# Kernel optimization log

Measured on AMD Instinct MI355X. Metric: run time of the kernel, lower is better.

Reference implementation:

```python
import jax, jax.numpy as jnp
import numpy as np
import math

DK = 768  # latent_size used for the scale (not the per-head dim, matching the original)

def setup_inputs() -> dict:
    key = jax.random.key(0)
    k1, k2, k3 = jax.random.split(key, 3)
    B, H, S, D = 4, 12, 2048, 64
    queries = jax.random.normal(k1, (B, H, S, D), dtype=jnp.float32)
    keys = jax.random.normal(k2, (B, H, S, D), dtype=jnp.float32)
    values = jax.random.normal(k3, (B, S, H, D), dtype=jnp.float32)  # note [B,S,H,D] layout
    return {"queries": queries, "keys": keys, "values": values}

def reference(queries, keys, values):
    # scores: [B,H,S,S]
    scores = jnp.einsum('bhqd,bhkd->bhqk', queries, keys) / math.sqrt(DK)
    probs = jax.nn.softmax(scores, axis=3)
    v = jnp.transpose(values, (0, 2, 1, 3))  # [B,S,H,D] -> [B,H,S,D]
    return jnp.einsum('bhqk,bhkd->bhqd', probs, v)
```

## Files before the change

kernel.cpp:

```cpp
#include <hip/hip_runtime.h>

#define SQ 2048
#define DH 64
#define NH 12
#define NBH 48
#define QTILE 64
#define KTILE 64
#define NITER (SQ / KTILE)
#define NQT (SQ / QTILE)

typedef short short8 __attribute__((ext_vector_type(8)));
typedef float f32x4 __attribute__((ext_vector_type(4)));
typedef int   i32x4 __attribute__((ext_vector_type(4)));
typedef int   i32x2 __attribute__((ext_vector_type(2)));

#define MFMA16(a, b, c) __builtin_amdgcn_mfma_f32_16x16x32_bf16(a, b, c, 0, 0, 0)

typedef __attribute__((address_space(1))) const void* gas_ptr;
typedef __attribute__((address_space(3))) void* las_ptr;

__device__ __forceinline__ void load_lds16(const void* g, void* l) {
    __builtin_amdgcn_global_load_lds((gas_ptr)g, (las_ptr)l, 16, 0, 0);
}

__device__ __forceinline__ short f2bf(float f) {
    union { float f; unsigned u; } v;
    v.f = f;
    unsigned r = v.u + 0x7FFFu + ((v.u >> 16) & 1u);
    return (short)(r >> 16);
}

#if defined(__has_builtin) && __has_builtin(__builtin_amdgcn_cvt_pk_bf16_f32)
typedef __bf16 bf16x2_t __attribute__((ext_vector_type(2)));
__device__ __forceinline__ unsigned pk2bf(float a, float b) {
    bf16x2_t v = __builtin_amdgcn_cvt_pk_bf16_f32(a, b);
    union { bf16x2_t v; unsigned u; } c; c.v = v; return c.u;
}
#else
__device__ __forceinline__ unsigned pk2bf(float a, float b) {
    union { float f; unsigned u; } x, y; x.f = a; y.f = b;
    unsigned ra = x.u + 0x7FFFu + ((x.u >> 16) & 1u);
    unsigned rb = y.u + 0x7FFFu + ((y.u >> 16) & 1u);
    return (ra >> 16) | (rb & 0xFFFF0000u);
}
#endif

__global__ __launch_bounds__(256)
void convert_k(const float* __restrict__ K, short* __restrict__ Kb) {
    const size_t i = (size_t)(blockIdx.x * 256 + threadIdx.x) * 8;
    f32x4 a = *(const f32x4*)&K[i];
    f32x4 b = *(const f32x4*)&K[i + 4];
    unsigned o[4] = { pk2bf(a[0], a[1]), pk2bf(a[2], a[3]),
                      pk2bf(b[0], b[1]), pk2bf(b[2], b[3]) };
    *(i32x4*)&Kb[i] = *(i32x4*)o;
}

__global__ __launch_bounds__(256)
void transpose_v(const float* __restrict__ V, short* __restrict__ Vt) {
    __shared__ float Ls[64][68];
    const int bx = blockIdx.x;
    const int st = bx & 31;
    const int bh = bx >> 5;
    const int b = bh / NH, h = bh % NH;
    const int s0 = st * 64;
    const float* src = V + ((size_t)b * SQ * NH + (size_t)h) * DH;
    const int dg = threadIdx.x & 15;
    const int sl = threadIdx.x >> 4;
    #pragma unroll
    for (int p = 0; p < 4; ++p) {
        const int row = p * 16 + sl;
        *(f32x4*)&Ls[row][dg * 4] =
            *(const f32x4*)&src[(size_t)(s0 + row) * (NH * DH) + dg * 4];
    }
    __syncthreads();
    const int dr = threadIdx.x >> 2;
    const int sc = (threadIdx.x & 3) * 16;
    unsigned out[8];
    #pragma unroll
    for (int jj = 0; jj < 8; ++jj)
        out[jj] = pk2bf(Ls[sc + 2 * jj][dr], Ls[sc + 2 * jj + 1][dr]);
    short* dst = Vt + (size_t)bh * DH * SQ + (size_t)dr * SQ + s0 + sc;
    *(i32x4*)(dst)     = *(i32x4*)&out[0];
    *(i32x4*)(dst + 8) = *(i32x4*)&out[4];
}

__global__ __launch_bounds__(256)
void attn_fused_kernel(const float* __restrict__ Q,
                       const short* __restrict__ Kb,
                       const short* __restrict__ Vtg,
                       float* __restrict__ O) {
    __shared__ short Ks[KTILE * DH];
    __shared__ short Vs[DH * KTILE];
    __shared__ short Ps[QTILE][72];

    const int tid  = threadIdx.x;
    const int lane = tid & 63;
    const int w    = tid >> 6;
    const int n    = lane & 15;
    const int quad = lane >> 4;
    const int nx   = n & 7;

    const int bx = blockIdx.x;
    const int qt = bx & (NQT - 1);
    const int bh = bx >> 5;
    const int q0 = qt * QTILE;

    const float* Qb  = Q   + (size_t)bh * SQ * DH;
    const short* Kbh = Kb  + (size_t)bh * SQ * DH;
    const short* Vbh = Vtg + (size_t)bh * DH * SQ;
    float*       Ob  = O   + (size_t)bh * SQ * DH;

    const float qscale = 0.03608439182435161f * 1.4426950408889634f;

    short8 qf[2];
    {
        const int qrow = q0 + 16 * w + n;
        #pragma unroll
        for (int c = 0; c < 2; ++c) {
            const float* src = Qb + (size_t)qrow * DH + 32 * c + 8 * quad;
            short8 f;
            #pragma unroll
            for (int j = 0; j < 8; ++j) f[j] = f2bf(src[j] * qscale);
            qf[c] = f;
        }
    }

    const int gk = (lane & 7) ^ (lane >> 3);
    const int rr = w * 8 + (lane >> 3);
    const short* kg0 = Kbh + (size_t)rr * DH + gk * 8;
    const short* kg1 = kg0 + 32 * DH;
    const short* vg0 = Vbh + (size_t)rr * SQ + gk * 8;
    const short* vg1 = vg0 + 32 * SQ;
    char* ksb = (char*)Ks;
    char* vsb = (char*)Vs;

    const short* kb0p = &Ks[n * DH + ((quad ^ nx) * 8)];
    const short* kb1p = &Ks[n * DH + (((4 + quad) ^ nx) * 8)];
    const short* vb0p = &Vs[n * DH + ((quad ^ nx) * 8)];
    const short* vb1p = &Vs[n * DH + (((4 + quad) ^ nx) * 8)];

    f32x4 o[4];
    #pragma unroll
    for (int dt = 0; dt < 4; ++dt) o[dt] = (f32x4){0.f, 0.f, 0.f, 0.f};
    float lp[4] = {0.f, 0.f, 0.f, 0.f};

    for (int it = 0; it < NITER; ++it) {
        const size_t ko = (size_t)it * (KTILE * DH);
        const size_t vo = (size_t)it * KTILE;
        load_lds16(kg0 + ko, ksb + w * 1024);
        load_lds16(kg1 + ko, ksb + 4096 + w * 1024);
        load_lds16(vg0 + vo, vsb + w * 1024);
        load_lds16(vg1 + vo, vsb + 4096 + w * 1024);
        __syncthreads();

        f32x4 s[4];
        #pragma unroll
        for (int c = 0; c < 4; ++c) {
            short8 kb0 = *(const short8*)(kb0p + c * 1024);
            short8 kb1 = *(const short8*)(kb1p + c * 1024);
            f32x4 acc = (f32x4){0.f, 0.f, 0.f, 0.f};
            acc = MFMA16(kb0, qf[0], acc);
            acc = MFMA16(kb1, qf[1], acc);
            s[c] = acc;
        }

        #pragma unroll
        for (int c = 0; c < 4; ++c) {
            float p0 = __builtin_amdgcn_exp2f(s[c][0]);
            float p1 = __builtin_amdgcn_exp2f(s[c][1]);
            float p2 = __builtin_amdgcn_exp2f(s[c][2]);
            float p3 = __builtin_amdgcn_exp2f(s[c][3]);
            lp[c] += (p0 + p1) + (p2 + p3);
            i32x2 w2 = { (int)pk2bf(p0, p1), (int)pk2bf(p2, p3) };
            *(i32x2*)&Ps[16 * w + n][16 * c + 4 * quad] = w2;
        }

        #pragma unroll
        for (int kc = 0; kc < 2; ++kc) {
            short8 pa = *(const short8*)&Ps[16 * w + n][32 * kc + 8 * quad];
            const short* vbp = kc ? vb1p : vb0p;
            #pragma unroll
            for (int dt = 0; dt < 4; ++dt) {
                short8 vb = *(const short8*)(vbp + dt * 1024);
                o[dt] = MFMA16(pa, vb, o[dt]);
            }
        }
        __syncthreads();
    }

    float v = (lp[0] + lp[1]) + (lp[2] + lp[3]);
    v += __shfl_xor(v, 16, 64);
    v += __shfl_xor(v, 32, 64);
    const float linv = 1.0f / v;

    float rl[4];
    #pragma unroll
    for (int r = 0; r < 4; ++r) rl[r] = __shfl(linv, 4 * quad + r, 64);

    #pragma unroll
    for (int dt = 0; dt < 4; ++dt)
        #pragma unroll
        for (int r = 0; r < 4; ++r) {
            const int q = q0 + 16 * w + 4 * quad + r;
            Ob[(size_t)q * DH + 16 * dt + n] = o[dt][r] * rl[r];
        }
}

extern "C" void kernel_launch(void* const* d_in, const int* in_sizes, int n_in,
                              void* d_out, int out_size, void* d_ws, size_t ws_size,
                              hipStream_t stream) {
    const float* Q = (const float*)d_in[0];
    const float* K = (const float*)d_in[1];
    const float* V = (const float*)d_in[2];
    float* O = (float*)d_out;

    short* Kb  = (short*)d_ws;
    short* Vtg = Kb + (size_t)NBH * SQ * DH;

    convert_k<<<dim3(NBH * SQ * DH / 8 / 256), dim3(256), 0, stream>>>(K, Kb);
    transpose_v<<<dim3(NBH * 32), dim3(256), 0, stream>>>(V, Vtg);
    attn_fused_kernel<<<dim3(NBH * NQT), dim3(256), 0, stream>>>(Q, Kb, Vtg, O);
}
```

Measured before the change: 190.7 us.

## Use 32x32x16 MFMA with 128-row query tiles in fused attention

Each wave now owns 32 query rows instead of 16, so one block covers 128 queries, and the score and PV products use the 32x32x16 bf16 MFMA. Fragment indexing, the LDS swizzle offsets, the row-sum reduction and the output write are rewritten for the 32x32 accumulator layout. The aim is to halve how often each K/V tile is loaded per query and to raise MFMA work per LDS read. In exchange the grid has half as many blocks and each thread holds larger accumulators, which may lower occupancy.

After: 185.1 us. -2.9%, faster.

```diff
diff --git a/kernel.cpp b/kernel.cpp
--- a/kernel.cpp
+++ b/kernel.cpp
@@ -4,17 +4,18 @@
 #define DH 64
 #define NH 12
 #define NBH 48
-#define QTILE 64
+#define QTILE 128
 #define KTILE 64
 #define NITER (SQ / KTILE)
 #define NQT (SQ / QTILE)
 
 typedef short short8 __attribute__((ext_vector_type(8)));
-typedef float f32x4 __attribute__((ext_vector_type(4)));
+typedef float f32x4  __attribute__((ext_vector_type(4)));
+typedef float f32x16 __attribute__((ext_vector_type(16)));
 typedef int   i32x4 __attribute__((ext_vector_type(4)));
 typedef int   i32x2 __attribute__((ext_vector_type(2)));
 
-#define MFMA16(a, b, c) __builtin_amdgcn_mfma_f32_16x16x32_bf16(a, b, c, 0, 0, 0)
+#define MFMA32(a, b, c) __builtin_amdgcn_mfma_f32_32x32x16_bf16(a, b, c, 0, 0, 0)
 
 typedef __attribute__((address_space(1))) const void* gas_ptr;
 typedef __attribute__((address_space(3))) void* las_ptr;
@@ -96,13 +97,13 @@
     const int tid  = threadIdx.x;
     const int lane = tid & 63;
     const int w    = tid >> 6;
-    const int n    = lane & 15;
-    const int quad = lane >> 4;
-    const int nx   = n & 7;
+    const int m31  = lane & 31;
+    const int hl   = lane >> 5;
+    const int l7   = lane & 7;
 
     const int bx = blockIdx.x;
     const int qt = bx & (NQT - 1);
-    const int bh = bx >> 5;
+    const int bh = bx >> 4;
     const int q0 = qt * QTILE;
 
     const float* Qb  = Q   + (size_t)bh * SQ * DH;
@@ -112,16 +113,16 @@
 
     const float qscale = 0.03608439182435161f * 1.4426950408889634f;
 
-    short8 qf[2];
+    short8 qf[4];
     {
-        const int qrow = q0 + 16 * w + n;
-        #pragma unroll
-        for (int c = 0; c < 2; ++c) {
-            const float* src = Qb + (size_t)qrow * DH + 32 * c + 8 * quad;
+        const int qrow = q0 + 32 * w + m31;
+        #pragma unroll
+        for (int s = 0; s < 4; ++s) {
+            const float* src = Qb + (size_t)qrow * DH + 16 * s + 8 * hl;
             short8 f;
             #pragma unroll
             for (int j = 0; j < 8; ++j) f[j] = f2bf(src[j] * qscale);
-            qf[c] = f;
+            qf[s] = f;
         }
     }
 
@@ -134,15 +135,15 @@
     char* ksb = (char*)Ks;
     char* vsb = (char*)Vs;
 
-    const short* kb0p = &Ks[n * DH + ((quad ^ nx) * 8)];
-    const short* kb1p = &Ks[n * DH + (((4 + quad) ^ nx) * 8)];
-    const short* vb0p = &Vs[n * DH + ((quad ^ nx) * 8)];
-    const short* vb1p = &Vs[n * DH + (((4 + quad) ^ nx) * 8)];
-
-    f32x4 o[4];
-    #pragma unroll
-    for (int dt = 0; dt < 4; ++dt) o[dt] = (f32x4){0.f, 0.f, 0.f, 0.f};
-    float lp[4] = {0.f, 0.f, 0.f, 0.f};
+    int koff[4];
+    #pragma unroll
+    for (int s = 0; s < 4; ++s) koff[s] = (((2 * s + hl) ^ l7) * 8);
+    const short* kbase = Ks + m31 * DH;
+    const short* vbase = Vs + m31 * DH;
+    short* prow = &Ps[32 * w + m31][0];
+
+    f32x16 o0 = {}, o1 = {};
+    float lp = 0.f;
 
     for (int it = 0; it < NITER; ++it) {
         const size_t ko = (size_t)it * (KTILE * DH);
@@ -153,57 +154,62 @@
         load_lds16(vg1 + vo, vsb + 4096 + w * 1024);
         __syncthreads();
 
-        f32x4 s[4];
-        #pragma unroll
-        for (int c = 0; c < 4; ++c) {
-            short8 kb0 = *(const short8*)(kb0p + c * 1024);
-            short8 kb1 = *(const short8*)(kb1p + c * 1024);
-            f32x4 acc = (f32x4){0.f, 0.f, 0.f, 0.f};
-            acc = MFMA16(kb0, qf[0], acc);
-            acc = MFMA16(kb1, qf[1], acc);
-            s[c] = acc;
-        }
-
-        #pragma unroll
-        for (int c = 0; c < 4; ++c) {
-            float p0 = __builtin_amdgcn_exp2f(s[c][0]);
-            float p1 = __builtin_amdgcn_exp2f(s[c][1]);
-            float p2 = __builtin_amdgcn_exp2f(s[c][2]);
-            float p3 = __builtin_amdgcn_exp2f(s[c][3]);
-            lp[c] += (p0 + p1) + (p2 + p3);
+        f32x16 s0 = {}, s1 = {};
+        #pragma unroll
+        for (int s = 0; s < 4; ++s) {
+            short8 ka0 = *(const short8*)(kbase + koff[s]);
+            short8 ka1 = *(const short8*)(kbase + 2048 + koff[s]);
+            s0 = MFMA32(ka0, qf[s], s0);
+            s1 = MFMA32(ka1, qf[s], s1);
+        }
+
+        #pragma unroll
+        for (int g = 0; g < 4; ++g) {
+            float p0 = __builtin_amdgcn_exp2f(s0[4 * g + 0]);
+            float p1 = __builtin_amdgcn_exp2f(s0[4 * g + 1]);
+            float p2 = __builtin_amdgcn_exp2f(s0[4 * g + 2]);
+            float p3 = __builtin_amdgcn_exp2f(s0[4 * g + 3]);
+            lp += (p0 + p1) + (p2 + p3);
             i32x2 w2 = { (int)pk2bf(p0, p1), (int)pk2bf(p2, p3) };
-            *(i32x2*)&Ps[16 * w + n][16 * c + 4 * quad] = w2;
-        }
-
-        #pragma unroll
-        for (int kc = 0; kc < 2; ++kc) {
-            short8 pa = *(const short8*)&Ps[16 * w + n][32 * kc + 8 * quad];
-            const short* vbp = kc ? vb1p : vb0p;
-            #pragma unroll
-            for (int dt = 0; dt < 4; ++dt) {
-                short8 vb = *(const short8*)(vbp + dt * 1024);
-                o[dt] = MFMA16(pa, vb, o[dt]);
-            }
+            *(i32x2*)(prow + 8 * g + 4 * hl) = w2;
+        }
+        #pragma unroll
+        for (int g = 0; g < 4; ++g) {
+            float p0 = __builtin_amdgcn_exp2f(s1[4 * g + 0]);
+            float p1 = __builtin_amdgcn_exp2f(s1[4 * g + 1]);
+            float p2 = __builtin_amdgcn_exp2f(s1[4 * g + 2]);
+            float p3 = __builtin_amdgcn_exp2f(s1[4 * g + 3]);
+            lp += (p0 + p1) + (p2 + p3);
+            i32x2 w2 = { (int)pk2bf(p0, p1), (int)pk2bf(p2, p3) };
+            *(i32x2*)(prow + 32 + 8 * g + 4 * hl) = w2;
+        }
+
+        #pragma unroll
+        for (int s = 0; s < 4; ++s) {
+            short8 pa  = *(const short8*)(prow + 16 * s + 8 * hl);
+            short8 vb0 = *(const short8*)(vbase + koff[s]);
+            short8 vb1 = *(const short8*)(vbase + 2048 + koff[s]);
+            o0 = MFMA32(pa, vb0, o0);
+            o1 = MFMA32(pa, vb1, o1);
         }
         __syncthreads();
     }
 
-    float v = (lp[0] + lp[1]) + (lp[2] + lp[3]);
-    v += __shfl_xor(v, 16, 64);
+    float v = lp;
     v += __shfl_xor(v, 32, 64);
     const float linv = 1.0f / v;
 
-    float rl[4];
-    #pragma unroll
-    for (int r = 0; r < 4; ++r) rl[r] = __shfl(linv, 4 * quad + r, 64);
-
-    #pragma unroll
-    for (int dt = 0; dt < 4; ++dt)
-        #pragma unroll
-        for (int r = 0; r < 4; ++r) {
-            const int q = q0 + 16 * w + 4 * quad + r;
-            Ob[(size_t)q * DH + 16 * dt + n] = o[dt][r] * rl[r];
-        }
+    #pragma unroll
+    for (int dt = 0; dt < 2; ++dt) {
+        const f32x16& o = dt ? o1 : o0;
+        #pragma unroll
+        for (int reg = 0; reg < 16; ++reg) {
+            const int qp = (reg & 3) + 8 * (reg >> 2) + 4 * hl;
+            const float rl = __shfl(linv, qp, 64);
+            const int q = q0 + 32 * w + qp;
+            Ob[(size_t)q * DH + 32 * dt + m31] = o[reg] * rl;
+        }
+    }
 }
 
 extern "C" void kernel_launch(void* const* d_in, const int* in_sizes, int n_in,
```
